# Kernel tuning notes

Measured on AMD Instinct MI355X. Metric: run time of the kernel, lower is better.

The kernel has to match this reference:

```python
import jax, jax.numpy as jnp
import numpy as np

STATE = 300
CAUSE = 40
PATCH = 16
N_PATCH = 4
GAMMA0 = 0.2


def _norm_cols(w):
    # torch: w / w.norm(dim=2, keepdim=True) on (1,1,r,c) -> normalize over rows
    return w / jnp.linalg.norm(w, axis=0, keepdims=True)[None, :][0]


def setup_inputs() -> dict:
    key = jax.random.key(0)
    kX, kU, kx0, kA, kB, kC = jax.random.split(key, 6)
    B, T = 256, 64
    X = jax.random.normal(kX, (B, N_PATCH, STATE, 1, T), dtype=jnp.float32)
    U = jax.random.normal(kU, (B, 1, CAUSE, 1, T), dtype=jnp.float32)
    x0 = jax.random.normal(kx0, (B, N_PATCH, STATE, 1), dtype=jnp.float32)
    # parameters: uniform then column-normalized over dim=2 (row axis), as in __init__
    A = jax.random.uniform(kA, (STATE, STATE), dtype=jnp.float32)
    A = A / jnp.linalg.norm(A, axis=0, keepdims=True)
    Bm = jax.random.uniform(kB, (STATE, CAUSE), dtype=jnp.float32)
    Bm = Bm / jnp.linalg.norm(Bm, axis=0, keepdims=True)
    C = jax.random.uniform(kC, (PATCH * PATCH, STATE), dtype=jnp.float32)
    C = C / jnp.linalg.norm(C, axis=0, keepdims=True)
    return {"X": X, "U": U, "x0": x0, "A": A, "Bm": Bm, "C": C}


def reference(X, U, x0, A, Bm, C):
    # X: (B, 4, 300, 1, T); U: (B, 1, 40, 1, T); x0: (B, 4, 300, 1)
    Bsz, npatch, _, _, T = X.shape
    # x_prev sequence: [x0, X[...,0], ..., X[...,T-2]]
    X_prev = jnp.concatenate([x0[..., None], X[..., :-1]], axis=-1)
    # X_pred[t] = A @ x_prev_t   -> (B, 4, 300, 1, T)
    X_pred = jnp.einsum('ij,bpjkt->bpikt', A, X_prev)
    # recon[t] = C @ x_t -> (B, 4, 256, 1, T)
    recon = jnp.einsum('ij,bpjkt->bpikt', C, X)
    # patch_to_image, vectorized over trailing T: grid 2x2 of 16x16 patches -> 32x32
    gs = int(np.sqrt(npatch))
    img = recon.reshape(Bsz, gs, gs, 1, PATCH, PATCH, T)
    img = img.transpose(0, 3, 1, 4, 2, 5, 6)
    vid_recon = img.reshape(Bsz, 1, gs * PATCH, gs * PATCH, T)
    # cause state: gamma0*(1+exp(-B@u))/2 * sum_p |x|
    Bu = jnp.einsum('ij,bojkt->boikt', Bm, U)           # (B,1,300,1,T)
    gamma = GAMMA0 * (1.0 + jnp.exp(-Bu)) * 0.5
    X_U = gamma * jnp.sum(jnp.abs(X), axis=1, keepdims=True)  # (B,1,300,1,T)
    return vid_recon, X_pred, X_U
```

## Files before the change

kernel.cpp:

```cpp
#include <hip/hip_runtime.h>

#define STATE  300
#define TDIM   64
#define NCAUSE 40
#define NP     4
#define KPAD   320
#define ROWB   (KPAD*2)
#define NROWS  33
#define LDS_HALF (NROWS*ROWB)
#define NT_A   19
#define NT_C   16
#define WS_NEEDED 716800u

typedef float f32x4 __attribute__((ext_vector_type(4)));
typedef short s16x8 __attribute__((ext_vector_type(8)));

static __device__ __forceinline__ ushort f2bf(float f) {
    uint x = __float_as_uint(f);
    x += 0x7fffu + ((x >> 16) & 1u);
    return (ushort)(x >> 16);
}
static __device__ __forceinline__ float bf2f(ushort u) {
    return __uint_as_float(((uint)u) << 16);
}

__global__ void prep_kernel(const float* __restrict__ A, const float* __restrict__ C,
                            ushort* __restrict__ ws) {
    const int it   = blockIdx.x;
    const int ks   = blockIdx.y;
    const int lane = threadIdx.x;
    const bool isA = (it < NT_A);
    const float* __restrict__ W = isA ? A : C;
    const int M   = isA ? STATE : 256;
    const int itl = isA ? it : it - NT_A;
    const int row = itl*16 + (lane & 15);
    const int k0  = ks*32 + (lane >> 4)*8;

    ushort hv[8], lv[8];
    #pragma unroll
    for (int j = 0; j < 8; ++j) {
        const int k = k0 + j;
        float v = 0.f;
        if (row < M && k < STATE) v = W[row*STATE + k];
        const ushort h = f2bf(v);
        hv[j] = h;
        lv[j] = f2bf(v - bf2f(h));
    }
    const int plane = (isA ? NT_A : NT_C)*10*64*8;
    ushort* hb = ws + (isA ? 0 : 2*NT_A*10*64*8) + ((itl*10 + ks)*64 + lane)*8;
    ushort* lb = hb + plane;
    #pragma unroll
    for (int j = 0; j < 8; ++j) { hb[j] = hv[j]; lb[j] = lv[j]; }
}

#define MFMA_(A_,B_,C_) __builtin_amdgcn_mfma_f32_16x16x32_bf16((A_),(B_),(C_),0,0,0)

static __device__ __forceinline__ s16x8 ldA(const ushort* __restrict__ base, int it, int ks, int lane) {
    return *(const s16x8*)(base + ((it*10 + ks)*64 + lane)*8);
}
static __device__ __forceinline__ void ldB(const char* Xs, int lr, int kbyte, s16x8& bh, s16x8& bl) {
    const int off = (lr*ROWB + kbyte) ^ ((lr & 7) << 4);
    bh = *(const s16x8*)(Xs + off);
    bl = *(const s16x8*)(Xs + off + LDS_HALF);
}

template<int PHOFF>
static __device__ __forceinline__ void gemm2(const char* Xs,
        const ushort* __restrict__ Wh, const ushort* __restrict__ Wl,
        int it0, int it1, int lane, int kg, int c,
        f32x4& a00, f32x4& a01, f32x4& a10, f32x4& a11) {
    #pragma unroll 2
    for (int ks = 0; ks < 10; ++ks) {
        const s16x8 ah0 = ldA(Wh, it0, ks, lane);
        const s16x8 al0 = ldA(Wl, it0, ks, lane);
        const s16x8 ah1 = ldA(Wh, it1, ks, lane);
        const s16x8 al1 = ldA(Wl, it1, ks, lane);
        const int kbyte = ks*64 + kg*16;
        s16x8 bh0, bl0, bh1, bl1;
        ldB(Xs, c + PHOFF,      kbyte, bh0, bl0);
        ldB(Xs, 16 + c + PHOFF, kbyte, bh1, bl1);
        a00 = MFMA_(ah0, bh0, a00); a00 = MFMA_(ah0, bl0, a00); a00 = MFMA_(al0, bh0, a00);
        a01 = MFMA_(ah0, bh1, a01); a01 = MFMA_(ah0, bl1, a01); a01 = MFMA_(al0, bh1, a01);
        a10 = MFMA_(ah1, bh0, a10); a10 = MFMA_(ah1, bl0, a10); a10 = MFMA_(al1, bh0, a10);
        a11 = MFMA_(ah1, bh1, a11); a11 = MFMA_(ah1, bl1, a11); a11 = MFMA_(al1, bh1, a11);
    }
}

template<int PHOFF>
static __device__ __forceinline__ void gemm1(const char* Xs,
        const ushort* __restrict__ Wh, const ushort* __restrict__ Wl,
        int it0, int lane, int kg, int c, f32x4& a00, f32x4& a01) {
    #pragma unroll 2
    for (int ks = 0; ks < 10; ++ks) {
        const s16x8 ah0 = ldA(Wh, it0, ks, lane);
        const s16x8 al0 = ldA(Wl, it0, ks, lane);
        const int kbyte = ks*64 + kg*16;
        s16x8 bh0, bl0, bh1, bl1;
        ldB(Xs, c + PHOFF,      kbyte, bh0, bl0);
        ldB(Xs, 16 + c + PHOFF, kbyte, bh1, bl1);
        a00 = MFMA_(ah0, bh0, a00); a00 = MFMA_(ah0, bl0, a00); a00 = MFMA_(al0, bh0, a00);
        a01 = MFMA_(ah0, bh1, a01); a01 = MFMA_(ah0, bl1, a01); a01 = MFMA_(al0, bh1, a01);
    }
}

__global__ __launch_bounds__(256, 3)
void pred_recon_mfma(const float* __restrict__ X, const float* __restrict__ x0,
                     const ushort* __restrict__ ws,
                     float* __restrict__ vid, float* __restrict__ Xpred) {
    __shared__ __align__(16) char Xs[2*LDS_HALF];
    const int bp   = blockIdx.x;
    const int th   = blockIdx.y;
    const int tid  = threadIdx.x;
    const int lane = tid & 63;
    const int w    = tid >> 6;

    const float* __restrict__ Xbp = X + (size_t)bp*(STATE*TDIM);
    {
        const int t_lo = tid & 31;
        const int kh   = tid >> 5;
        const int tg   = th*32 + t_lo;
        const int lr   = t_lo + 1;
        const int sw   = (lr & 7) << 4;
        #pragma unroll 1
        for (int i = 0; i < 10; ++i) {
            const int k4 = kh + 8*i;
            if (k4 < 75) {
                const int k = k4*4;
                const float v0 = Xbp[(k+0)*TDIM + tg];
                const float v1 = Xbp[(k+1)*TDIM + tg];
                const float v2 = Xbp[(k+2)*TDIM + tg];
                const float v3 = Xbp[(k+3)*TDIM + tg];
                const ushort h0 = f2bf(v0), h1 = f2bf(v1), h2 = f2bf(v2), h3 = f2bf(v3);
                uint2 hp, lp;
                hp.x = (uint)h0 | ((uint)h1 << 16);
                hp.y = (uint)h2 | ((uint)h3 << 16);
                lp.x = (uint)f2bf(v0 - bf2f(h0)) | ((uint)f2bf(v1 - bf2f(h1)) << 16);
                lp.y = (uint)f2bf(v2 - bf2f(h2)) | ((uint)f2bf(v3 - bf2f(h3)) << 16);
                const int off = (lr*ROWB + k*2) ^ sw;
                *(uint2*)(Xs + off)            = hp;
                *(uint2*)(Xs + off + LDS_HALF) = lp;
            }
        }
    }
    if (th == 0) {
        const float* __restrict__ x0bp = x0 + (size_t)bp*STATE;
        for (int k = tid; k < STATE; k += 256) {
            const float v = x0bp[k];
            const ushort h = f2bf(v);
            *(ushort*)(Xs + k*2)            = h;
            *(ushort*)(Xs + k*2 + LDS_HALF) = f2bf(v - bf2f(h));
        }
    } else {
        for (int k = tid; k < STATE; k += 256) {
            const float v = Xbp[k*TDIM + 31];
            const ushort h = f2bf(v);
            *(ushort*)(Xs + k*2)            = h;
            *(ushort*)(Xs + k*2 + LDS_HALF) = f2bf(v - bf2f(h));
        }
    }
    for (int idx = tid; idx < 2*NROWS; idx += 256) {
        const int plane = idx & 1, lr = idx >> 1;
        char* base = Xs + plane*LDS_HALF;
        const int sw = (lr & 7) << 4;
        uint2 z; z.x = 0u; z.y = 0u;
        #pragma unroll
        for (int j = 0; j < 5; ++j)
            *(uint2*)(base + ((lr*ROWB + 600 + j*8) ^ sw)) = z;
    }
    __syncthreads();

    const int c  = lane & 15;
    const int kg = lane >> 4;
    const int tbase = th*32;
    const ushort* __restrict__ Af_h = ws;
    const ushort* __restrict__ Af_l = Af_h + NT_A*10*64*8;
    const ushort* __restrict__ Cf_h = Af_l + NT_A*10*64*8;
    const ushort* __restrict__ Cf_l = Cf_h + NT_C*10*64*8;

    const int ps = (w*9 < NT_A) ? w*9 : NT_A;
    const int pe = (ps + 9 < NT_A) ? ps + 9 : NT_A;
    const int rs = (w < 3) ? 0 : 8;
    const int re = (w < 2) ? 0 : (w - 1)*8;

    {
        float* __restrict__ outp = Xpred + (size_t)bp*(STATE*TDIM);
        int it = ps;
        for (; it + 1 < pe; it += 2) {
            f32x4 a00 = {0,0,0,0}, a01 = {0,0,0,0}, a10 = {0,0,0,0}, a11 = {0,0,0,0};
            gemm2<0>(Xs, Af_h, Af_l, it, it+1, lane, kg, c, a00, a01, a10, a11);
            #pragma unroll
            for (int r = 0; r < 4; ++r) {
                const int row0 = it*16 + kg*4 + r;
                const int row1 = row0 + 16;
                outp[row0*TDIM + tbase + c]      = a00[r];
                outp[row0*TDIM + tbase + 16 + c] = a01[r];
                if (row1 < STATE) {
                    outp[row1*TDIM + tbase + c]      = a10[r];
                    outp[row1*TDIM + tbase + 16 + c] = a11[r];
                }
            }
        }
        if (it < pe) {
            f32x4 a00 = {0,0,0,0}, a01 = {0,0,0,0};
            gemm1<0>(Xs, Af_h, Af_l, it, lane, kg, c, a00, a01);
            #pragma unroll
            for (int r = 0; r < 4; ++r) {
                const int row = it*16 + kg*4 + r;
                if (row < STATE) {
                    outp[row*TDIM + tbase + c]      = a00[r];
                    outp[row*TDIM + tbase + 16 + c] = a01[r];
                }
            }
        }
    }

    if (rs < re) {
        const int b = bp >> 2, p = bp & 3, gr = p >> 1, gc = p & 1;
        float* __restrict__ vb = vid + (size_t)b*(32*32*TDIM)
                                     + (size_t)(gr*16)*(32*TDIM)
                                     + (size_t)(gc*16)*TDIM;
        for (int it = rs; it + 1 < re + 1; it += 2) {
            f32x4 a00 = {0,0,0,0}, a01 = {0,0,0,0}, a10 = {0,0,0,0}, a11 = {0,0,0,0};
            gemm2<1>(Xs, Cf_h, Cf_l, it, it+1, lane, kg, c, a00, a01, a10, a11);
            #pragma unroll
            for (int r = 0; r < 4; ++r) {
                const int pc = kg*4 + r;
                float* vr0 = vb + (it  )*(32*TDIM) + pc*TDIM + tbase;
                float* vr1 = vb + (it+1)*(32*TDIM) + pc*TDIM + tbase;
                vr0[c]      = a00[r];
                vr0[16 + c] = a01[r];
                vr1[c]      = a10[r];
                vr1[16 + c] = a11[r];
            }
        }
    }
}

__global__ __launch_bounds__(256)
void xu_kernel(const float* __restrict__ X, const float* __restrict__ U,
               const float* __restrict__ Bm, float* __restrict__ XU) {
    __shared__ float gl[60*68];
    const int b    = blockIdx.y;
    const int sg   = blockIdx.x;
    const int tid  = threadIdx.x;
    const int lane = tid & 63;
    const int w    = __builtin_amdgcn_readfirstlane(tid >> 6);

    const float* __restrict__ Ub = U + (size_t)b*(NCAUSE*TDIM);
    float u[40];
    #pragma unroll
    for (int k = 0; k < 40; ++k) u[k] = Ub[k*TDIM + lane];

    const int sbase = sg*60;
    const int s0    = w*15;
    #pragma unroll 1
    for (int r = 0; r < 15; ++r) {
        const float* __restrict__ brow = Bm + (size_t)(sbase + s0 + r)*NCAUSE;
        float bu = 0.f;
        #pragma unroll
        for (int q = 0; q < 10; ++q) {
            const float4 m = *(const float4*)(brow + q*4);
            bu += m.x*u[4*q] + m.y*u[4*q+1] + m.z*u[4*q+2] + m.w*u[4*q+3];
        }
        gl[(s0 + r)*68 + lane] = 0.1f*(1.f + __expf(-bu));
    }
    __syncthreads();

    const float* __restrict__ Xb  = X  + (size_t)b*(NP*STATE*TDIM);
    float* __restrict__ XUb       = XU + (size_t)b*(STATE*TDIM);
    #pragma unroll 1
    for (int idx = tid; idx < 60*16; idx += 256) {
        const int sp = idx >> 4, t4 = idx & 15;
        const int s  = sbase + sp;
        const float4 g = *(const float4*)(gl + sp*68 + t4*4);
        float4 a; a.x = 0.f; a.y = 0.f; a.z = 0.f; a.w = 0.f;
        #pragma unroll
        for (int p = 0; p < NP; ++p) {
            const float4 xv = *(const float4*)(Xb + ((size_t)p*STATE + s)*TDIM + t4*4);
            a.x += fabsf(xv.x); a.y += fabsf(xv.y); a.z += fabsf(xv.z); a.w += fabsf(xv.w);
        }
        float4 o; o.x = g.x*a.x; o.y = g.y*a.y; o.z = g.z*a.z; o.w = g.w*a.w;
        *(float4*)(XUb + (size_t)s*TDIM + t4*4) = o;
    }
}

__global__ __launch_bounds__(256, 2)
void pred_recon_f32(const float* __restrict__ X, const float* __restrict__ x0,
                    const float* __restrict__ A, const float* __restrict__ C,
                    float* __restrict__ vid, float* __restrict__ Xpred) {
    __shared__ float Xsf[STATE*65];
    const int bp = blockIdx.x, tid = threadIdx.x;
    const float* Xbp = X + (size_t)bp*(STATE*TDIM);
    const float* x0bp = x0 + (size_t)bp*STATE;
    for (int idx = tid; idx < STATE*65; idx += 256) {
        const int k = idx/65, tp = idx - k*65;
        Xsf[idx] = (tp == 0) ? x0bp[k] : Xbp[k*TDIM + (tp-1)];
    }
    __syncthreads();
    const int t = tid & 63, rg = tid >> 6;
    float* outp = Xpred + (size_t)bp*(STATE*TDIM);
    for (int chunk = 0; chunk < 15; ++chunk) {
        const int i0 = rg*75 + chunk*5;
        float acc[5] = {0,0,0,0,0};
        for (int k4 = 0; k4 < STATE/4; ++k4) {
            const int kb = k4*4;
            const float x0v = Xsf[(kb+0)*65 + t], x1v = Xsf[(kb+1)*65 + t];
            const float x2v = Xsf[(kb+2)*65 + t], x3v = Xsf[(kb+3)*65 + t];
            #pragma unroll
            for (int r = 0; r < 5; ++r) {
                const float4 a = *(const float4*)(A + (size_t)(i0+r)*STATE + kb);
                acc[r] += a.x*x0v + a.y*x1v + a.z*x2v + a.w*x3v;
            }
        }
        #pragma unroll
        for (int r = 0; r < 5; ++r) outp[(i0+r)*TDIM + t] = acc[r];
    }
    const int b = bp >> 2, p = bp & 3, gr = p >> 1, gc = p & 1;
    float* vb = vid + (size_t)b*(32*32*TDIM) + (size_t)(gr*16)*(32*TDIM) + (size_t)(gc*16)*TDIM;
    for (int chunk = 0; chunk < 16; ++chunk) {
        const int i0 = rg*64 + chunk*4;
        float acc[4] = {0,0,0,0};
        for (int k4 = 0; k4 < STATE/4; ++k4) {
            const int kb = k4*4;
            const float x0v = Xsf[(kb+0)*65 + (t+1)], x1v = Xsf[(kb+1)*65 + (t+1)];
            const float x2v = Xsf[(kb+2)*65 + (t+1)], x3v = Xsf[(kb+3)*65 + (t+1)];
            #pragma unroll
            for (int r = 0; r < 4; ++r) {
                const float4 cc = *(const float4*)(C + (size_t)(i0+r)*STATE + kb);
                acc[r] += cc.x*x0v + cc.y*x1v + cc.z*x2v + cc.w*x3v;
            }
        }
        #pragma unroll
        for (int r = 0; r < 4; ++r) {
            const int i = i0 + r;
            vb[(i >> 4)*(32*TDIM) + (i & 15)*TDIM + t] = acc[r];
        }
    }
}

extern "C" void kernel_launch(void* const* d_in, const int* in_sizes, int n_in,
                              void* d_out, int out_size, void* d_ws, size_t ws_size,
                              hipStream_t stream) {
    const float* X  = (const float*)d_in[0];
    const float* U  = (const float*)d_in[1];
    const float* x0 = (const float*)d_in[2];
    const float* A  = (const float*)d_in[3];
    const float* Bm = (const float*)d_in[4];
    const float* C  = (const float*)d_in[5];

    float* out   = (float*)d_out;
    float* vid   = out;
    float* Xpred = out + 16777216;
    float* XU    = out + 16777216 + 19660800;

    if (ws_size >= WS_NEEDED) {
        ushort* wsu = (ushort*)d_ws;
        hipLaunchKernelGGL(prep_kernel, dim3(NT_A + NT_C, 10), dim3(64), 0, stream,
                           A, C, wsu);
        hipLaunchKernelGGL(pred_recon_mfma, dim3(256*NP, 2), dim3(256), 0, stream,
                           X, x0, wsu, vid, Xpred);
    } else {
        hipLaunchKernelGGL(pred_recon_f32, dim3(256*NP), dim3(256), 0, stream,
                           X, x0, A, C, vid, Xpred);
    }
    hipLaunchKernelGGL(xu_kernel, dim3(5, 256), dim3(256), 0, stream,
                       X, U, Bm, XU);
}
```

Before: 317.3 us.

## Software-pipeline GEMM operand loads and vectorize X staging into LDS

The GEMM inner loops now prefetch the next k-step's A fragments from global memory and B fragments from LDS while the MFMAs of the current step run, so load latency overlaps with matrix math. The X tile staging now issues float4 global loads over three batched iterations before converting to bf16 hi/lo pairs, replacing the earlier scalar strided loads. The x0/prev-column row is also packed four values per thread. The cost is higher register pressure from the double-buffered fragments, which could reduce occupancy under the launch bound of 3 blocks per CU, plus one redundant final load at k-step 9.

```diff
diff --git a/kernel.cpp b/kernel.cpp
--- a/kernel.cpp
+++ b/kernel.cpp
@@ -23,6 +23,9 @@
 static __device__ __forceinline__ float bf2f(ushort u) {
     return __uint_as_float(((uint)u) << 16);
 }
+static __device__ __forceinline__ uint pack2(float a, float b) {
+    return (uint)f2bf(a) | ((uint)f2bf(b) << 16);
+}
 
 __global__ void prep_kernel(const float* __restrict__ A, const float* __restrict__ C,
                             ushort* __restrict__ ws) {
@@ -69,20 +72,26 @@
         const ushort* __restrict__ Wh, const ushort* __restrict__ Wl,
         int it0, int it1, int lane, int kg, int c,
         f32x4& a00, f32x4& a01, f32x4& a10, f32x4& a11) {
+    s16x8 ah0 = ldA(Wh, it0, 0, lane), al0 = ldA(Wl, it0, 0, lane);
+    s16x8 ah1 = ldA(Wh, it1, 0, lane), al1 = ldA(Wl, it1, 0, lane);
+    s16x8 bh0, bl0, bh1, bl1;
+    ldB(Xs, c + PHOFF,      kg*16, bh0, bl0);
+    ldB(Xs, 16 + c + PHOFF, kg*16, bh1, bl1);
     #pragma unroll 2
     for (int ks = 0; ks < 10; ++ks) {
-        const s16x8 ah0 = ldA(Wh, it0, ks, lane);
-        const s16x8 al0 = ldA(Wl, it0, ks, lane);
-        const s16x8 ah1 = ldA(Wh, it1, ks, lane);
-        const s16x8 al1 = ldA(Wl, it1, ks, lane);
-        const int kbyte = ks*64 + kg*16;
-        s16x8 bh0, bl0, bh1, bl1;
-        ldB(Xs, c + PHOFF,      kbyte, bh0, bl0);
-        ldB(Xs, 16 + c + PHOFF, kbyte, bh1, bl1);
+        const int ksn = (ks < 9) ? ks + 1 : 9;
+        s16x8 nh0 = ldA(Wh, it0, ksn, lane), nl0 = ldA(Wl, it0, ksn, lane);
+        s16x8 nh1 = ldA(Wh, it1, ksn, lane), nl1 = ldA(Wl, it1, ksn, lane);
+        const int kbn = ksn*64 + kg*16;
+        s16x8 mh0, ml0, mh1, ml1;
+        ldB(Xs, c + PHOFF,      kbn, mh0, ml0);
+        ldB(Xs, 16 + c + PHOFF, kbn, mh1, ml1);
         a00 = MFMA_(ah0, bh0, a00); a00 = MFMA_(ah0, bl0, a00); a00 = MFMA_(al0, bh0, a00);
         a01 = MFMA_(ah0, bh1, a01); a01 = MFMA_(ah0, bl1, a01); a01 = MFMA_(al0, bh1, a01);
         a10 = MFMA_(ah1, bh0, a10); a10 = MFMA_(ah1, bl0, a10); a10 = MFMA_(al1, bh0, a10);
         a11 = MFMA_(ah1, bh1, a11); a11 = MFMA_(ah1, bl1, a11); a11 = MFMA_(al1, bh1, a11);
+        ah0 = nh0; al0 = nl0; ah1 = nh1; al1 = nl1;
+        bh0 = mh0; bl0 = ml0; bh1 = mh1; bl1 = ml1;
     }
 }
 
@@ -90,16 +99,22 @@
 static __device__ __forceinline__ void gemm1(const char* Xs,
         const ushort* __restrict__ Wh, const ushort* __restrict__ Wl,
         int it0, int lane, int kg, int c, f32x4& a00, f32x4& a01) {
+    s16x8 ah0 = ldA(Wh, it0, 0, lane), al0 = ldA(Wl, it0, 0, lane);
+    s16x8 bh0, bl0, bh1, bl1;
+    ldB(Xs, c + PHOFF,      kg*16, bh0, bl0);
+    ldB(Xs, 16 + c + PHOFF, kg*16, bh1, bl1);
     #pragma unroll 2
     for (int ks = 0; ks < 10; ++ks) {
-        const s16x8 ah0 = ldA(Wh, it0, ks, lane);
-        const s16x8 al0 = ldA(Wl, it0, ks, lane);
-        const int kbyte = ks*64 + kg*16;
-        s16x8 bh0, bl0, bh1, bl1;
-        ldB(Xs, c + PHOFF,      kbyte, bh0, bl0);
-        ldB(Xs, 16 + c + PHOFF, kbyte, bh1, bl1);
+        const int ksn = (ks < 9) ? ks + 1 : 9;
+        s16x8 nh0 = ldA(Wh, it0, ksn, lane), nl0 = ldA(Wl, it0, ksn, lane);
+        const int kbn = ksn*64 + kg*16;
+        s16x8 mh0, ml0, mh1, ml1;
+        ldB(Xs, c + PHOFF,      kbn, mh0, ml0);
+        ldB(Xs, 16 + c + PHOFF, kbn, mh1, ml1);
         a00 = MFMA_(ah0, bh0, a00); a00 = MFMA_(ah0, bl0, a00); a00 = MFMA_(al0, bh0, a00);
         a01 = MFMA_(ah0, bh1, a01); a01 = MFMA_(ah0, bl1, a01); a01 = MFMA_(al0, bh1, a01);
+        ah0 = nh0; al0 = nl0;
+        bh0 = mh0; bl0 = ml0; bh1 = mh1; bl1 = ml1;
     }
 }
 
@@ -116,47 +131,67 @@
 
     const float* __restrict__ Xbp = X + (size_t)bp*(STATE*TDIM);
     {
-        const int t_lo = tid & 31;
-        const int kh   = tid >> 5;
-        const int tg   = th*32 + t_lo;
-        const int lr   = t_lo + 1;
-        const int sw   = (lr & 7) << 4;
-        #pragma unroll 1
-        for (int i = 0; i < 10; ++i) {
-            const int k4 = kh + 8*i;
-            if (k4 < 75) {
-                const int k = k4*4;
-                const float v0 = Xbp[(k+0)*TDIM + tg];
-                const float v1 = Xbp[(k+1)*TDIM + tg];
-                const float v2 = Xbp[(k+2)*TDIM + tg];
-                const float v3 = Xbp[(k+3)*TDIM + tg];
-                const ushort h0 = f2bf(v0), h1 = f2bf(v1), h2 = f2bf(v2), h3 = f2bf(v3);
-                uint2 hp, lp;
-                hp.x = (uint)h0 | ((uint)h1 << 16);
-                hp.y = (uint)h2 | ((uint)h3 << 16);
-                lp.x = (uint)f2bf(v0 - bf2f(h0)) | ((uint)f2bf(v1 - bf2f(h1)) << 16);
-                lp.y = (uint)f2bf(v2 - bf2f(h2)) | ((uint)f2bf(v3 - bf2f(h3)) << 16);
-                const int off = (lr*ROWB + k*2) ^ sw;
-                *(uint2*)(Xs + off)            = hp;
-                *(uint2*)(Xs + off + LDS_HALF) = lp;
-            }
-        }
-    }
-    if (th == 0) {
-        const float* __restrict__ x0bp = x0 + (size_t)bp*STATE;
-        for (int k = tid; k < STATE; k += 256) {
-            const float v = x0bp[k];
-            const ushort h = f2bf(v);
-            *(ushort*)(Xs + k*2)            = h;
-            *(ushort*)(Xs + k*2 + LDS_HALF) = f2bf(v - bf2f(h));
-        }
-    } else {
-        for (int k = tid; k < STATE; k += 256) {
-            const float v = Xbp[k*TDIM + 31];
-            const ushort h = f2bf(v);
-            *(ushort*)(Xs + k*2)            = h;
-            *(ushort*)(Xs + k*2 + LDS_HALF) = f2bf(v - bf2f(h));
-        }
+        float4 r[3][4];
+        int k4v[3], t0v[3];
+        bool act[3];
+        #pragma unroll
+        for (int itr = 0; itr < 3; ++itr) {
+            const int idx = tid + itr*256;
+            act[itr] = (idx < 600);
+            const int k4 = idx >> 3;
+            const int t0 = (idx & 7)*4;
+            k4v[itr] = k4; t0v[itr] = t0;
+            if (act[itr]) {
+                const float* src = Xbp + (size_t)(k4*4)*TDIM + th*32 + t0;
+                r[itr][0] = *(const float4*)(src + 0*TDIM);
+                r[itr][1] = *(const float4*)(src + 1*TDIM);
+                r[itr][2] = *(const float4*)(src + 2*TDIM);
+                r[itr][3] = *(const float4*)(src + 3*TDIM);
+            }
+        }
+        #pragma unroll
+        for (int itr = 0; itr < 3; ++itr) {
+            if (act[itr]) {
+                const int kbyte = k4v[itr]*8;
+                #pragma unroll
+                for (int i = 0; i < 4; ++i) {
+                    const float v0 = ((const float*)&r[itr][0])[i];
+                    const float v1 = ((const float*)&r[itr][1])[i];
+                    const float v2 = ((const float*)&r[itr][2])[i];
+                    const float v3 = ((const float*)&r[itr][3])[i];
+                    uint2 hp, lp;
+                    hp.x = pack2(v0, v1);
+                    hp.y = pack2(v2, v3);
+                    lp.x = pack2(v0 - bf2f((ushort)(hp.x & 0xffff)),
+                                 v1 - bf2f((ushort)(hp.x >> 16)));
+                    lp.y = pack2(v2 - bf2f((ushort)(hp.y & 0xffff)),
+                                 v3 - bf2f((ushort)(hp.y >> 16)));
+                    const int lr  = t0v[itr] + i + 1;
+                    const int off = (lr*ROWB + kbyte) ^ ((lr & 7) << 4);
+                    *(uint2*)(Xs + off)            = hp;
+                    *(uint2*)(Xs + off + LDS_HALF) = lp;
+                }
+            }
+        }
+    }
+    if (tid < 75) {
+        float v0, v1, v2, v3;
+        if (th == 0) {
+            const float4 v = *(const float4*)(x0 + (size_t)bp*STATE + tid*4);
+            v0 = v.x; v1 = v.y; v2 = v.z; v3 = v.w;
+        } else {
+            const float* src = Xbp + (size_t)(tid*4)*TDIM + 31;
+            v0 = src[0*TDIM]; v1 = src[1*TDIM]; v2 = src[2*TDIM]; v3 = src[3*TDIM];
+        }
+        uint2 hp, lp;
+        hp.x = pack2(v0, v1);
+        hp.y = pack2(v2, v3);
+        lp.x = pack2(v0 - bf2f((ushort)(hp.x & 0xffff)),
+                     v1 - bf2f((ushort)(hp.x >> 16)));
+        lp.y = pack2(v2 - bf2f((ushort)(hp.y & 0xffff)),
+                     v3 - bf2f((ushort)(hp.y >> 16)));
+        *(uint2*)(Xs + tid*8)            = hp;
+        *(uint2*)(Xs + tid*8 + LDS_HALF) = lp;
     }
     for (int idx = tid; idx < 2*NROWS; idx += 256) {
         const int plane = idx & 1, lr = idx >> 1;
```

New measurement: 338.4 us. 6.7% more time.
